# Optimization experiments

Hardware: AMD Instinct MI355X
Metric: run time of the kernel (lower is better)

## Reference

```python
import jax, jax.numpy as jnp
import numpy as np

N = 100000
E = 1600000
IN_DIM = 128
HID = 128
OUT_DIM = 64
ORDER = 4


def setup_inputs() -> dict:
    key = jax.random.key(0)
    ks = jax.random.split(key, 10)
    x = jax.random.normal(ks[0], (N, IN_DIM), dtype=jnp.float32)
    edge_index = jax.random.randint(ks[1], (2, E), 0, N, dtype=jnp.int64)
    gen_edge_index = jax.random.randint(ks[2], (2, E), 0, N, dtype=jnp.int64)
    s = 1.0 / np.sqrt(IN_DIM)
    w_orig = jax.random.normal(ks[3], (ORDER + 1, IN_DIM, HID), dtype=jnp.float32) * s
    b_orig = jax.random.normal(ks[4], (ORDER + 1, HID), dtype=jnp.float32) * s
    w_aug = jax.random.normal(ks[5], (ORDER + 1, IN_DIM, HID), dtype=jnp.float32) * s
    b_aug = jax.random.normal(ks[6], (ORDER + 1, HID), dtype=jnp.float32) * s
    fusion_weight = jnp.ones((2,), dtype=jnp.float32)
    clf_w = jax.random.normal(ks[7], (HID, OUT_DIM), dtype=jnp.float32) / np.sqrt(HID)
    clf_b = jax.random.normal(ks[8], (OUT_DIM,), dtype=jnp.float32) / np.sqrt(HID)
    return {"x": x, "edge_index": edge_index, "gen_edge_index": gen_edge_index,
            "w_orig": w_orig, "b_orig": b_orig, "w_aug": w_aug, "b_aug": b_aug,
            "fusion_weight": fusion_weight, "clf_w": clf_w, "clf_b": clf_b}


def _beta_wavelet(x, edge_index, W, b, num_nodes):
    # add self loops
    loop = jnp.arange(num_nodes, dtype=edge_index.dtype)
    row = jnp.concatenate([edge_index[0], loop])
    col = jnp.concatenate([edge_index[1], loop])
    # symmetric normalization D^{-1/2} A D^{-1/2}
    deg = jax.ops.segment_sum(jnp.ones_like(col, dtype=x.dtype), col, num_segments=num_nodes)
    dinv = jnp.where(deg > 0, deg ** -0.5, 0.0)
    norm = dinv[row] * dinv[col]  # [E+N]
    out = x @ W[0] + b[0]
    Tx = x
    for i in range(1, ORDER + 1):
        msg = norm[:, None] * Tx[row]                      # gather + scale [E+N, D]
        Tx = jax.ops.segment_sum(msg, col, num_segments=num_nodes)  # scatter_add
        out = out + Tx @ W[i] + b[i]
    return jax.nn.relu(out)


def reference(x, edge_index, gen_edge_index, w_orig, b_orig, w_aug, b_aug, fusion_weight, clf_w, clf_b):
    num_nodes = x.shape[0]
    h_orig = _beta_wavelet(x, edge_index, w_orig, b_orig, num_nodes)
    h_aug = _beta_wavelet(x, gen_edge_index, w_aug, b_aug, num_nodes)
    w = jax.nn.softmax(fusion_weight)
    h_final = w[0] * h_orig + w[1] * h_aug
    return h_final @ clf_w + clf_b
```

## Files before the change

### kernel.cpp

```cpp
#include <hip/hip_runtime.h>

#define N_NODES 100000
#define NPAD    100096
#define NE      1600000
#define DIM     128
#define ODIM    64
#define NORDER  4
#define NB      391
#define PB_EDGES 16384
#define PB_BLKS  98

typedef _Float16 h8 __attribute__((ext_vector_type(8)));
typedef float f4 __attribute__((ext_vector_type(4)));

__device__ __forceinline__ float2 up2(unsigned p) {
    union { unsigned u; _Float16 h[2]; } c; c.u = p;
    return make_float2((float)c.h[0], (float)c.h[1]);
}
__device__ __forceinline__ unsigned pk2(float x, float y) {
    union { unsigned u; _Float16 h[2]; } c;
    c.h[0] = (_Float16)x; c.h[1] = (_Float16)y;
    return c.u;
}
__device__ __forceinline__ unsigned short f2hbits(float x) {
    union { _Float16 h; unsigned short s; } c;
    c.h = (_Float16)x;
    return c.s;
}
__device__ __forceinline__ float h2f(unsigned short s) {
    union { unsigned short u; _Float16 h; } c;
    c.u = s;
    return (float)c.h;
}

__global__ __launch_bounds__(256) void hist_edges(const int* __restrict__ e0,
                                                  const int* __restrict__ e1,
                                                  int* __restrict__ bhist) {
    __shared__ int lh[NB];
    int t = threadIdx.x;
    int g = blockIdx.x >= 782;
    int blk = g ? (blockIdx.x - 782) : blockIdx.x;
    const int* colp = (g ? e1 : e0) + NE;
    int* bh = bhist + g * NB;
    for (int i = t; i < NB; i += 256) lh[i] = 0;
    __syncthreads();
    int base = blk * 2048 + t;
#pragma unroll
    for (int j = 0; j < 8; ++j) {
        int e = base + j * 256;
        if (e < NE) atomicAdd(&lh[colp[e] >> 8], 1);
    }
    __syncthreads();
    for (int i = t; i < NB; i += 256) if (lh[i]) atomicAdd(&bh[i], lh[i]);
}

__global__ void wave_scan(const int* __restrict__ in,
                          int* __restrict__ oexcl,
                          int* __restrict__ ocur,
                          int n) {
    int wv = threadIdx.x >> 6, lane = threadIdx.x & 63;
    if (wv >= 2) return;
    const int* I = in + wv * n;
    int* O = oexcl + wv * (n + 1);
    int* C = ocur + wv * n;
    int carry = 0;
    for (int base = 0; base < n; base += 64) {
        int i = base + lane;
        int v = (i < n) ? I[i] : 0;
        int s = v;
#pragma unroll
        for (int off = 1; off < 64; off <<= 1) {
            int x = __shfl_up(s, off, 64);
            if (lane >= off) s += x;
        }
        int excl = carry + s - v;
        if (i < n) {
            O[i] = excl;
            C[i] = excl;
        }
        carry += __shfl(s, 63, 64);
    }
    if (lane == 0) O[n] = carry;
}

__global__ __launch_bounds__(1024) void part_edges(const int* __restrict__ e0,
                                                   const int* __restrict__ e1,
                                                   int* __restrict__ bcursor,
                                                   unsigned* __restrict__ pairs) {
    __shared__ int lh[NB];
    __shared__ int lpos[NB];
    int t = threadIdx.x;
    int g = blockIdx.x >= PB_BLKS;
    int blk = g ? (blockIdx.x - PB_BLKS) : blockIdx.x;
    const int* rowp = (g ? e1 : e0);
    const int* colp = rowp + NE;
    int* bc = bcursor + g * NB;
    unsigned* pr = pairs + (size_t)g * NE;
    for (int i = t; i < NB; i += 1024) lh[i] = 0;
    __syncthreads();
    int base = blk * PB_EDGES + t;
    int rank[16];
    short bk[16];
    unsigned char lcv[16];
#pragma unroll
    for (int j = 0; j < 16; ++j) {
        int e = base + j * 1024;
        rank[j] = -1;
        if (e < NE) {
            int c = colp[e];
            bk[j] = (short)(c >> 8);
            lcv[j] = (unsigned char)(c & 255);
            rank[j] = atomicAdd(&lh[c >> 8], 1);
        }
    }
    __syncthreads();
    for (int i = t; i < NB; i += 1024) {
        int n = lh[i];
        lpos[i] = n ? atomicAdd(&bc[i], n) : 0;
    }
    __syncthreads();
#pragma unroll
    for (int j = 0; j < 16; ++j) {
        int e = base + j * 1024;
        if (e < NE) {
            int b = bk[j];
            pr[lpos[b] + rank[j]] = ((unsigned)rowp[e] << 8) | lcv[j];
        }
    }
}

__global__ __launch_bounds__(256) void bucket_csr(const unsigned* __restrict__ pairs,
                                                  const int* __restrict__ boff,
                                                  int* __restrict__ ptrv,
                                                  float* __restrict__ dinv,
                                                  int* __restrict__ srcv) {
    __shared__ int lcnt[256];
    __shared__ int lbase[256];
    int t = threadIdx.x;
    int g = blockIdx.x >= NB;
    int b = g ? (blockIdx.x - NB) : blockIdx.x;
    const unsigned* pr = pairs + (size_t)g * NE;
    const int* bo = boff + g * (NB + 1);
    int* pv = ptrv + g * (N_NODES + 1);
    float* dv = dinv + g * N_NODES;
    int* sv = srcv + (size_t)g * NE;
    lcnt[t] = 0;
    __syncthreads();
    int s = bo[b], e = bo[b + 1];
    for (int i = s + t; i < e; i += 256)
        atomicAdd(&lcnt[pr[i] & 255u], 1);
    __syncthreads();
    int v = lcnt[t];
    lbase[t] = v;
    __syncthreads();
    for (int off = 1; off < 256; off <<= 1) {
        int x = (t >= off) ? lbase[t - off] : 0;
        __syncthreads();
        lbase[t] += x;
        __syncthreads();
    }
    int node = (b << 8) + t;
    int gbase = s + lbase[t] - v;
    lbase[t] = gbase;
    lcnt[t] = 0;
    if (node < N_NODES) {
        pv[node] = gbase;
        dv[node] = rsqrtf((float)(v + 1));
    }
    if (b == 0 && g == 0 && t == 0) ptrv[N_NODES] = NE;
    if (b == 0 && g == 1 && t == 0) ptrv[2 * N_NODES + 1] = NE;
    __syncthreads();
    for (int i = s + t; i < e; i += 256) {
        unsigned pk = pr[i];
        int lc = (int)(pk & 255u);
        int pos = lbase[lc] + atomicAdd(&lcnt[lc], 1);
        sv[pos] = (int)(pk >> 8);
    }
}

__global__ __launch_bounds__(256) void s0cast(const float* __restrict__ x,
                                              const float* __restrict__ dinv,
                                              unsigned* __restrict__ S0o,
                                              unsigned* __restrict__ S0a) {
    int idx = blockIdx.x * 256 + threadIdx.x;
    if (idx >= NPAD * 64) return;
    int m = idx >> 6, u = idx & 63;
    if (m < N_NODES) {
        int e = (m << 7) + u * 2;
        float a = x[e], b = x[e + 1];
        float d0 = dinv[m];
        float d1 = dinv[N_NODES + m];
        S0o[idx] = pk2(d0 * a, d0 * b);
        S0a[idx] = pk2(d1 * a, d1 * b);
    } else {
        S0o[idx] = 0u;
        S0a[idx] = 0u;
    }
}

__global__ __launch_bounds__(256) void wcast(const float* __restrict__ Wo,
                                             const float* __restrict__ Wa,
                                             const float* __restrict__ cw,
                                             const float* __restrict__ bO,
                                             const float* __restrict__ bA,
                                             const float* __restrict__ fw,
                                             unsigned short* __restrict__ Wt,
                                             float* __restrict__ params) {
    int idx = blockIdx.x * 256 + threadIdx.x;
    if (idx >= 2 * 5 * DIM * DIM + ODIM * DIM) return;
    if (idx < 258) {
        if (idx < 2) {
            float f0 = fw[0], f1 = fw[1];
            float mx = fmaxf(f0, f1);
            float e0 = expf(f0 - mx), e1 = expf(f1 - mx);
            params[idx] = (idx == 0 ? e0 : e1) / (e0 + e1);
        } else if (idx < 130) {
            int n = idx - 2;
            float s = 0.f;
            for (int i = 0; i <= NORDER; ++i) s += bO[i * DIM + n];
            params[idx] = s;
        } else {
            int n = idx - 130;
            float s = 0.f;
            for (int i = 0; i <= NORDER; ++i) s += bA[i * DIM + n];
            params[idx] = s;
        }
    }
    if (idx < 2 * 5 * DIM * DIM) {
        int g   = idx / (5 * DIM * DIM);
        int rem = idx % (5 * DIM * DIM);
        int i   = rem / (DIM * DIM);
        int r2  = rem % (DIM * DIM);
        int k8  = r2 >> 10;
        int n   = (r2 >> 3) & 127;
        int k7  = r2 & 7;
        int k   = k8 * 8 + k7;
        const float* W = g ? Wa : Wo;
        Wt[idx] = f2hbits(W[(i * DIM + k) * DIM + n]);
    } else {
        int j = idx - 2 * 5 * DIM * DIM;
        int n = j >> 7, k = j & 127;
        Wt[idx] = f2hbits(cw[k * ODIM + n]);
    }
}

template<int SIN>
__global__ __launch_bounds__(256) void propagate(const unsigned* __restrict__ Tin,
                                                 unsigned* __restrict__ Tout,
                                                 const int* __restrict__ ptrv,
                                                 const int* __restrict__ srcv,
                                                 const float* __restrict__ dinv) {
    int gid  = blockIdx.x * 256 + threadIdx.x;
    int lane = threadIdx.x & 63;
    int v    = __builtin_amdgcn_readfirstlane(gid >> 6);
    if (v >= N_NODES) return;
    float dv = dinv[v];
    float2 self = up2(Tin[(size_t)v * SIN + lane]);
    float ax = self.x, ay = self.y;
    int beg = ptrv[v], end = ptrv[v + 1];
    for (int k = beg; k < end; k += 16) {
        int u[16];
#pragma unroll
        for (int j = 0; j < 16; ++j) {
            int e  = k + j;
            int su = srcv[e < NE ? e : (NE - 1)];
            u[j]   = (e < end) ? su : N_NODES;
        }
        unsigned tw[16];
#pragma unroll
        for (int j = 0; j < 16; ++j)
            tw[j] = Tin[(size_t)((unsigned)u[j] * SIN) + lane];
#pragma unroll
        for (int j = 0; j < 16; ++j) {
            float2 t = up2(tw[j]);
            ax += t.x; ay += t.y;
        }
    }
    float s2 = dv * dv;
    Tout[(size_t)v * 256 + lane] = pk2(s2 * ax, s2 * ay);
}

__global__ __launch_bounds__(256, 2) void gemmH0(
        const unsigned short* __restrict__ A0,
        const unsigned short* __restrict__ A,
        const unsigned short* __restrict__ Wt,
        const float* __restrict__ params,
        const float* __restrict__ dinv,
        unsigned short* __restrict__ H0) {
    int t = threadIdx.x;
    int lane = t & 63, wv = t >> 6;
    int m0 = blockIdx.x * 128 + wv * 32;
    int l15 = lane & 15, q = lane >> 4;
    float sw0 = params[0];
    float bs[8];
#pragma unroll
    for (int nt = 0; nt < 8; ++nt) bs[nt] = params[2 + nt * 16 + l15];

    f4 acc[2][8];
#pragma unroll
    for (int mt = 0; mt < 2; ++mt)
#pragma unroll
        for (int nt = 0; nt < 8; ++nt) acc[mt][nt] = (f4)(0.f);

#pragma unroll
    for (int i = 0; i < 5; ++i) {
        const unsigned short* WtI = Wt + (size_t)i * DIM * DIM;
        const unsigned short* Ai = (i == 0) ? A0 : (A + (size_t)(i - 1) * DIM);
        const int rs = (i == 0) ? DIM : 512;
        h8 af[2][4];
#pragma unroll
        for (int mt = 0; mt < 2; ++mt)
#pragma unroll
            for (int kc = 0; kc < 4; ++kc)
                af[mt][kc] = *(const h8*)(Ai + (size_t)(m0 + mt * 16 + l15) * rs
                                             + (kc * 4 + q) * 8);
#pragma unroll
        for (int kc = 0; kc < 4; ++kc) {
            int c = kc * 4 + q;
#pragma unroll
            for (int nt = 0; nt < 8; ++nt) {
                h8 bf = *(const h8*)(WtI + (size_t)(c * 128 + nt * 16 + l15) * 8);
                acc[0][nt] = __builtin_amdgcn_mfma_f32_16x16x32_f16(af[0][kc], bf, acc[0][nt], 0, 0, 0);
                acc[1][nt] = __builtin_amdgcn_mfma_f32_16x16x32_f16(af[1][kc], bf, acc[1][nt], 0, 0, 0);
            }
        }
    }
#pragma unroll
    for (int mt = 0; mt < 2; ++mt) {
        float rd[4];
#pragma unroll
        for (int r = 0; r < 4; ++r) {
            int row = m0 + mt * 16 + q * 4 + r;
            rd[r] = 1.0f / dinv[row < N_NODES ? row : (N_NODES - 1)];
        }
#pragma unroll
        for (int nt = 0; nt < 8; ++nt) {
#pragma unroll
            for (int r = 0; r < 4; ++r) {
                int row = m0 + mt * 16 + q * 4 + r;
                H0[(size_t)row * DIM + nt * 16 + l15] =
                    f2hbits(sw0 * fmaxf(rd[r] * acc[mt][nt][r] + bs[nt], 0.f));
            }
        }
    }
}

__global__ __launch_bounds__(256, 2) void gemm_fused2(
        const unsigned short* __restrict__ A0,
        const unsigned short* __restrict__ A,
        const unsigned short* __restrict__ Wt,
        const unsigned short* __restrict__ H0,
        const float* __restrict__ params,
        const float* __restrict__ dinv,
        const unsigned short* __restrict__ clfWt,
        const float* __restrict__ clfB,
        float* __restrict__ out) {
    __shared__ unsigned short Hl[DIM * 132];
    int t = threadIdx.x;
    int lane = t & 63, wv = t >> 6;
    int mb = blockIdx.x * 128;
    int m0 = mb + wv * 32;
    int l15 = lane & 15, q = lane >> 4;
    float sw1 = params[1];
    float bs[8];
#pragma unroll
    for (int nt = 0; nt < 8; ++nt) bs[nt] = params[130 + nt * 16 + l15];

    f4 acc[2][8];
#pragma unroll
    for (int mt = 0; mt < 2; ++mt)
#pragma unroll
        for (int nt = 0; nt < 8; ++nt) acc[mt][nt] = (f4)(0.f);

#pragma unroll
    for (int i = 0; i < 5; ++i) {
        const unsigned short* WtI = Wt + (size_t)i * DIM * DIM;
        const unsigned short* Ai = (i == 0) ? A0 : (A + (size_t)(i - 1) * DIM);
        const int rs = (i == 0) ? DIM : 512;
        h8 af[2][4];
#pragma unroll
        for (int mt = 0; mt < 2; ++mt)
#pragma unroll
            for (int kc = 0; kc < 4; ++kc)
                af[mt][kc] = *(const h8*)(Ai + (size_t)(m0 + mt * 16 + l15) * rs
                                             + (kc * 4 + q) * 8);
#pragma unroll
        for (int kc = 0; kc < 4; ++kc) {
            int c = kc * 4 + q;
#pragma unroll
            for (int nt = 0; nt < 8; ++nt) {
                h8 bf = *(const h8*)(WtI + (size_t)(c * 128 + nt * 16 + l15) * 8);
                acc[0][nt] = __builtin_amdgcn_mfma_f32_16x16x32_f16(af[0][kc], bf, acc[0][nt], 0, 0, 0);
                acc[1][nt] = __builtin_amdgcn_mfma_f32_16x16x32_f16(af[1][kc], bf, acc[1][nt], 0, 0, 0);
            }
        }
    }

#pragma unroll
    for (int j = 0; j < 8; ++j) {
        int chunk = t + j * 256;
        int row = chunk >> 4, c8 = chunk & 15;
        *(h8*)&Hl[row * 132 + c8 * 8] =
            *(const h8*)&H0[(size_t)(mb + row) * DIM + c8 * 8];
    }
    __syncthreads();

#pragma unroll
    for (int mt = 0; mt < 2; ++mt) {
        float rd[4];
#pragma unroll
        for (int r = 0; r < 4; ++r) {
            int row = m0 + mt * 16 + q * 4 + r;
            rd[r] = 1.0f / dinv[row < N_NODES ? row : (N_NODES - 1)];
        }
#pragma unroll
        for (int nt = 0; nt < 8; ++nt) {
            int col = nt * 16 + l15;
#pragma unroll
            for (int r = 0; r < 4; ++r) {
                int lrow = wv * 32 + mt * 16 + q * 4 + r;
                float h = sw1 * fmaxf(rd[r] * acc[mt][nt][r] + bs[nt], 0.f)
                        + h2f(Hl[lrow * 132 + col]);
                Hl[lrow * 132 + col] = f2hbits(h);
            }
        }
    }
    __syncthreads();

    f4 o[2][4];
#pragma unroll
    for (int mt = 0; mt < 2; ++mt)
#pragma unroll
        for (int n2 = 0; n2 < 4; ++n2) o[mt][n2] = (f4)(0.f);
#pragma unroll
    for (int kc = 0; kc < 4; ++kc) {
        int c = kc * 4 + q;
        h8 ha[2];
#pragma unroll
        for (int mt = 0; mt < 2; ++mt)
            ha[mt] = *(const h8*)&Hl[(wv * 32 + mt * 16 + l15) * 132 + c * 8];
#pragma unroll
        for (int n2 = 0; n2 < 4; ++n2) {
            h8 bf = *(const h8*)&clfWt[(size_t)(n2 * 16 + l15) * DIM + c * 8];
            o[0][n2] = __builtin_amdgcn_mfma_f32_16x16x32_f16(ha[0], bf, o[0][n2], 0, 0, 0);
            o[1][n2] = __builtin_amdgcn_mfma_f32_16x16x32_f16(ha[1], bf, o[1][n2], 0, 0, 0);
        }
    }
#pragma unroll
    for (int mt = 0; mt < 2; ++mt)
#pragma unroll
        for (int n2 = 0; n2 < 4; ++n2) {
            int col = n2 * 16 + l15;
            float cbv = clfB[col];
#pragma unroll
            for (int r = 0; r < 4; ++r) {
                int row = m0 + mt * 16 + q * 4 + r;
                if (row < N_NODES) out[(size_t)row * ODIM + col] = o[mt][n2][r] + cbv;
            }
        }
}

extern "C" void kernel_launch(void* const* d_in, const int* in_sizes, int n_in,
                              void* d_out, int out_size, void* d_ws, size_t ws_size,
                              hipStream_t stream) {
    const float* x   = (const float*)d_in[0];
    const int*   ei  = (const int*)d_in[1];
    const int*   gi  = (const int*)d_in[2];
    const float* w_o = (const float*)d_in[3];
    const float* b_o = (const float*)d_in[4];
    const float* w_a = (const float*)d_in[5];
    const float* b_a = (const float*)d_in[6];
    const float* fw  = (const float*)d_in[7];
    const float* cw  = (const float*)d_in[8];
    const float* cb  = (const float*)d_in[9];
    float* out = (float*)d_out;

    char* p = (char*)d_ws;
    auto alloc = [&](size_t bytes) {
        void* r = (void*)p;
        p += (bytes + 255) & ~(size_t)255;
        return r;
    };
    unsigned* Tbig = (unsigned*)alloc((size_t)NPAD * 256 * 4);
    unsigned* S0o  = (unsigned*)alloc((size_t)NPAD * 64 * 4);
    unsigned* S0a  = (unsigned*)alloc((size_t)NPAD * 64 * 4);
    unsigned short* H0 = (unsigned short*)alloc((size_t)NPAD * DIM * 2);
    unsigned short* Wt = (unsigned short*)alloc(((size_t)2 * 5 * DIM * DIM + ODIM * DIM) * 2);
    float* params = (float*)alloc(258 * 4);
    float* dinv  = (float*)alloc((size_t)2 * N_NODES * 4);
    unsigned* pairs = (unsigned*)alloc((size_t)2 * NE * 4);
    int* csr_src = (int*)alloc((size_t)2 * NE * 4);
    int* csr_ptr = (int*)alloc((size_t)2 * (N_NODES + 1) * 4);
    int* bhist   = (int*)alloc((size_t)2 * NB * 4);
    int* boff    = (int*)alloc((size_t)2 * (NB + 1) * 4);
    int* bcursor = (int*)alloc((size_t)2 * NB * 4);

    const int gP  = (N_NODES * 64 + 255) / 256;
    const int gX  = (NPAD * 64 + 255) / 256;
    const int gW  = (2 * 5 * DIM * DIM + ODIM * DIM + 255) / 256;
    const int gM  = NPAD / 128;

    hipMemsetAsync(Tbig + (size_t)N_NODES * 256, 0,
                   (size_t)(NPAD - N_NODES) * 256 * 4, stream);
    hipMemsetAsync(bhist, 0, (size_t)2 * NB * 4, stream);

    wcast<<<gW, 256, 0, stream>>>(w_o, w_a, cw, b_o, b_a, fw, Wt, params);

    hist_edges<<<2 * 782, 256, 0, stream>>>(ei, gi, bhist);
    wave_scan<<<1, 128, 0, stream>>>(bhist, boff, bcursor, NB);
    part_edges<<<2 * PB_BLKS, 1024, 0, stream>>>(ei, gi, bcursor, pairs);
    bucket_csr<<<2 * NB, 256, 0, stream>>>(pairs, boff, csr_ptr, dinv, csr_src);

    s0cast<<<gX, 256, 0, stream>>>(x, dinv, S0o, S0a);

    propagate<64><<<gP, 256, 0, stream>>>(S0o, Tbig, csr_ptr, csr_src, dinv);
    propagate<256><<<gP, 256, 0, stream>>>(Tbig, Tbig + 64, csr_ptr, csr_src, dinv);
    propagate<256><<<gP, 256, 0, stream>>>(Tbig + 64, Tbig + 128, csr_ptr, csr_src, dinv);
    propagate<256><<<gP, 256, 0, stream>>>(Tbig + 128, Tbig + 192, csr_ptr, csr_src, dinv);
    gemmH0<<<gM, 256, 0, stream>>>((const unsigned short*)S0o, (const unsigned short*)Tbig,
                                   Wt, params, dinv, H0);

    {
        const int* pv = csr_ptr + (N_NODES + 1);
        const int* sv = csr_src + (size_t)NE;
        const float* dv = dinv + (size_t)N_NODES;
        propagate<64><<<gP, 256, 0, stream>>>(S0a, Tbig, pv, sv, dv);
        propagate<256><<<gP, 256, 0, stream>>>(Tbig, Tbig + 64, pv, sv, dv);
        propagate<256><<<gP, 256, 0, stream>>>(Tbig + 64, Tbig + 128, pv, sv, dv);
        propagate<256><<<gP, 256, 0, stream>>>(Tbig + 128, Tbig + 192, pv, sv, dv);
    }
    gemm_fused2<<<gM, 256, 0, stream>>>((const unsigned short*)S0a,
                                        (const unsigned short*)Tbig,
                                        Wt + (size_t)5 * DIM * DIM,
                                        H0, params, dinv + N_NODES,
                                        Wt + (size_t)2 * 5 * DIM * DIM, cb, out);
}
```

Before: 899.8 us.

## Double-buffer weight tiles in LDS via async global-to-LDS loads in fused GEMMs

Both MFMA GEMM kernels now stage each order's 128x128 fp16 weight tile into a double-buffered LDS array using global_load_lds async copies, prefetching the next order's weights and A fragments while computing the current one. Previously B fragments were read directly from global memory inside the inner MFMA loop. The fused kernel reuses the LDS buffer for the H tile and reads H0 directly from global memory instead of staging it. This raises LDS use to 64KB per block, which may reduce occupancy below the requested two blocks per CU, and it adds barriers per order.

```diff
diff --git a/kernel.cpp b/kernel.cpp
--- a/kernel.cpp
+++ b/kernel.cpp
@@ -31,6 +31,10 @@
     union { unsigned short u; _Float16 h; } c;
     c.u = s;
     return (float)c.h;
+}
+__device__ __forceinline__ void async_cp16(const void* g, void* l) {
+    __builtin_amdgcn_global_load_lds((const __attribute__((address_space(1))) void*)g,
+                                     (__attribute__((address_space(3))) void*)l, 16, 0, 0);
 }
 
 __global__ __launch_bounds__(256) void hist_edges(const int* __restrict__ e0,
@@ -287,6 +291,7 @@
         const float* __restrict__ params,
         const float* __restrict__ dinv,
         unsigned short* __restrict__ H0) {
+    __shared__ unsigned short Bl[2][DIM * DIM];
     int t = threadIdx.x;
     int lane = t & 63, wv = t >> 6;
     int m0 = blockIdx.x * 128 + wv * 32;
@@ -302,28 +307,50 @@
 #pragma unroll
         for (int nt = 0; nt < 8; ++nt) acc[mt][nt] = (f4)(0.f);
 
+    h8 af[2][2][4];
+
+#pragma unroll
+    for (int c = 0; c < 8; ++c) {
+        int ci = c * 4 + wv;
+        async_cp16(Wt + ci * 512 + lane * 8, &Bl[0][ci * 512]);
+    }
+#pragma unroll
+    for (int mt = 0; mt < 2; ++mt)
+#pragma unroll
+        for (int kc = 0; kc < 4; ++kc)
+            af[0][mt][kc] = *(const h8*)(A0 + (size_t)(m0 + mt * 16 + l15) * DIM
+                                            + (kc * 4 + q) * 8);
+    __syncthreads();
+
 #pragma unroll
     for (int i = 0; i < 5; ++i) {
-        const unsigned short* WtI = Wt + (size_t)i * DIM * DIM;
-        const unsigned short* Ai = (i == 0) ? A0 : (A + (size_t)(i - 1) * DIM);
-        const int rs = (i == 0) ? DIM : 512;
-        h8 af[2][4];
-#pragma unroll
-        for (int mt = 0; mt < 2; ++mt)
-#pragma unroll
-            for (int kc = 0; kc < 4; ++kc)
-                af[mt][kc] = *(const h8*)(Ai + (size_t)(m0 + mt * 16 + l15) * rs
-                                             + (kc * 4 + q) * 8);
+        if (i < 4) {
+            const unsigned short* WtN = Wt + (size_t)(i + 1) * DIM * DIM;
+#pragma unroll
+            for (int c = 0; c < 8; ++c) {
+                int ci = c * 4 + wv;
+                async_cp16(WtN + ci * 512 + lane * 8, &Bl[(i & 1) ^ 1][ci * 512]);
+            }
+            const unsigned short* AiN = A + (size_t)i * DIM;
+#pragma unroll
+            for (int mt = 0; mt < 2; ++mt)
+#pragma unroll
+                for (int kc = 0; kc < 4; ++kc)
+                    af[(i & 1) ^ 1][mt][kc] =
+                        *(const h8*)(AiN + (size_t)(m0 + mt * 16 + l15) * 512
+                                        + (kc * 4 + q) * 8);
+        }
 #pragma unroll
         for (int kc = 0; kc < 4; ++kc) {
             int c = kc * 4 + q;
 #pragma unroll
             for (int nt = 0; nt < 8; ++nt) {
-                h8 bf = *(const h8*)(WtI + (size_t)(c * 128 + nt * 16 + l15) * 8);
-                acc[0][nt] = __builtin_amdgcn_mfma_f32_16x16x32_f16(af[0][kc], bf, acc[0][nt], 0, 0, 0);
-                acc[1][nt] = __builtin_amdgcn_mfma_f32_16x16x32_f16(af[1][kc], bf, acc[1][nt], 0, 0, 0);
-            }
-        }
+                h8 bf = *(const h8*)&Bl[i & 1][(size_t)(c * 128 + nt * 16 + l15) * 8];
+                acc[0][nt] = __builtin_amdgcn_mfma_f32_16x16x32_f16(af[i & 1][0][kc], bf, acc[0][nt], 0, 0, 0);
+                acc[1][nt] = __builtin_amdgcn_mfma_f32_16x16x32_f16(af[i & 1][1][kc], bf, acc[1][nt], 0, 0, 0);
+            }
+        }
+        if (i < 4) __syncthreads();
     }
 #pragma unroll
     for (int mt = 0; mt < 2; ++mt) {
@@ -355,11 +382,11 @@
         const unsigned short* __restrict__ clfWt,
         const float* __restrict__ clfB,
         float* __restrict__ out) {
-    __shared__ unsigned short Hl[DIM * 132];
+    __shared__ unsigned short Bl[2][DIM * DIM];
+    unsigned short* Hl = &Bl[0][0];
     int t = threadIdx.x;
     int lane = t & 63, wv = t >> 6;
-    int mb = blockIdx.x * 128;
-    int m0 = mb + wv * 32;
+    int m0 = blockIdx.x * 128 + wv * 32;
     int l15 = lane & 15, q = lane >> 4;
     float sw1 = params[1];
     float bs[8];
@@ -372,38 +399,51 @@
 #pragma unroll
         for (int nt = 0; nt < 8; ++nt) acc[mt][nt] = (f4)(0.f);
 
+    h8 af[2][2][4];
+
+#pragma unroll
+    for (int c = 0; c < 8; ++c) {
+        int ci = c * 4 + wv;
+        async_cp16(Wt + ci * 512 + lane * 8, &Bl[0][ci * 512]);
+    }
+#pragma unroll
+    for (int mt = 0; mt < 2; ++mt)
+#pragma unroll
+        for (int kc = 0; kc < 4; ++kc)
+            af[0][mt][kc] = *(const h8*)(A0 + (size_t)(m0 + mt * 16 + l15) * DIM
+                                            + (kc * 4 + q) * 8);
+    __syncthreads();
+
 #pragma unroll
     for (int i = 0; i < 5; ++i) {
-        const unsigned short* WtI = Wt + (size_t)i * DIM * DIM;
-        const unsigned short* Ai = (i == 0) ? A0 : (A + (size_t)(i - 1) * DIM);
-        const int rs = (i == 0) ? DIM : 512;
-        h8 af[2][4];
-#pragma unroll
-        for (int mt = 0; mt < 2; ++mt)
-#pragma unroll
-            for (int kc = 0; kc < 4; ++kc)
-                af[mt][kc] = *(const h8*)(Ai + (size_t)(m0 + mt * 16 + l15) * rs
-                                             + (kc * 4 + q) * 8);
+        if (i < 4) {
+            const unsigned short* WtN = Wt + (size_t)(i + 1) * DIM * DIM;
+#pragma unroll
+            for (int c = 0; c < 8; ++c) {
+                int ci = c * 4 + wv;
+                async_cp16(WtN + ci * 512 + lane * 8, &Bl[(i & 1) ^ 1][ci * 512]);
+            }
+            const unsigned short* AiN = A + (size_t)i * DIM;
+#pragma unroll
+            for (int mt = 0; mt < 2; ++mt)
+#pragma unroll
+                for (int kc = 0; kc < 4; ++kc)
+                    af[(i & 1) ^ 1][mt][kc] =
+                        *(const h8*)(AiN + (size_t)(m0 + mt * 16 + l15) * 512
+                                        + (kc * 4 + q) * 8);
+        }
 #pragma unroll
         for (int kc = 0; kc < 4; ++kc) {
             int c = kc * 4 + q;
 #pragma unroll
             for (int nt = 0; nt < 8; ++nt) {
-                h8 bf = *(const h8*)(WtI + (size_t)(c * 128 + nt * 16 + l15) * 8);
-                acc[0][nt] = __builtin_amdgcn_mfma_f32_16x16x32_f16(af[0][kc], bf, acc[0][nt], 0, 0, 0);
-                acc[1][nt] = __builtin_amdgcn_mfma_f32_16x16x32_f16(af[1][kc], bf, acc[1][nt], 0, 0, 0);
-            }
-        }
-    }
-
-#pragma unroll
-    for (int j = 0; j < 8; ++j) {
-        int chunk = t + j * 256;
-        int row = chunk >> 4, c8 = chunk & 15;
-        *(h8*)&Hl[row * 132 + c8 * 8] =
-            *(const h8*)&H0[(size_t)(mb + row) * DIM + c8 * 8];
-    }
-    __syncthreads();
+                h8 bf = *(const h8*)&Bl[i & 1][(size_t)(c * 128 + nt * 16 + l15) * 8];
+                acc[0][nt] = __builtin_amdgcn_mfma_f32_16x16x32_f16(af[i & 1][0][kc], bf, acc[0][nt], 0, 0, 0);
+                acc[1][nt] = __builtin_amdgcn_mfma_f32_16x16x32_f16(af[i & 1][1][kc], bf, acc[1][nt], 0, 0, 0);
+            }
+        }
+        __syncthreads();
+    }
 
 #pragma unroll
     for (int mt = 0; mt < 2; ++mt) {
@@ -419,8 +459,9 @@
 #pragma unroll
             for (int r = 0; r < 4; ++r) {
                 int lrow = wv * 32 + mt * 16 + q * 4 + r;
+                int grow = m0 + mt * 16 + q * 4 + r;
                 float h = sw1 * fmaxf(rd[r] * acc[mt][nt][r] + bs[nt], 0.f)
-                        + h2f(Hl[lrow * 132 + col]);
+                        + h2f(H0[(size_t)grow * DIM + col]);
                 Hl[lrow * 132 + col] = f2hbits(h);
             }
         }
```

Result: faster. 785.7 us (-12.7%).

## Batch both graphs' propagation per launch and stage GEMM weights in LDS

Applied to the files above, without the earlier changes.

When the workspace is large enough, each propagation order now runs for the original and the augmented graph in a single launch, with a separate T buffer per graph and the pairs scratch aliased onto the second T buffer. This halves the number of propagation launches and doubles the blocks per wave of work. Both GEMM kernels now copy each weight slice into shared memory with async global-to-LDS loads, and gemmH0 occupancy is raised to 3. The host memsets move into existing kernels, and gemm_fused2 reads H0 directly from global memory. The extra barriers and the doubled buffer footprint could raise cache pressure.

```diff
diff --git a/kernel.cpp b/kernel.cpp
--- a/kernel.cpp
+++ b/kernel.cpp
@@ -9,9 +9,11 @@
 #define NB      391
 #define PB_EDGES 16384
 #define PB_BLKS  98
+#define GPB     25000
 
 typedef _Float16 h8 __attribute__((ext_vector_type(8)));
 typedef float f4 __attribute__((ext_vector_type(4)));
+typedef unsigned u4v __attribute__((ext_vector_type(4)));
 
 __device__ __forceinline__ float2 up2(unsigned p) {
     union { unsigned u; _Float16 h[2]; } c; c.u = p;
@@ -31,6 +33,10 @@
     union { unsigned short u; _Float16 h; } c;
     c.u = s;
     return (float)c.h;
+}
+__device__ __forceinline__ void async_cp16(const void* g, void* l) {
+    __builtin_amdgcn_global_load_lds((const __attribute__((address_space(1))) void*)g,
+                                     (__attribute__((address_space(3))) void*)l, 16, 0, 0);
 }
 
 __global__ __launch_bounds__(256) void hist_edges(const int* __restrict__ e0,
@@ -181,7 +187,9 @@
 __global__ __launch_bounds__(256) void s0cast(const float* __restrict__ x,
                                               const float* __restrict__ dinv,
                                               unsigned* __restrict__ S0o,
-                                              unsigned* __restrict__ S0a) {
+                                              unsigned* __restrict__ S0a,
+                                              unsigned* __restrict__ To,
+                                              unsigned* __restrict__ Ta) {
     int idx = blockIdx.x * 256 + threadIdx.x;
     if (idx >= NPAD * 64) return;
     int m = idx >> 6, u = idx & 63;
@@ -195,6 +203,9 @@
     } else {
         S0o[idx] = 0u;
         S0a[idx] = 0u;
+        u4v z = (u4v)(0u);
+        *(u4v*)&To[(size_t)m * 256 + u * 4] = z;
+        *(u4v*)&Ta[(size_t)m * 256 + u * 4] = z;
     }
 }
 
@@ -205,9 +216,11 @@
                                              const float* __restrict__ bA,
                                              const float* __restrict__ fw,
                                              unsigned short* __restrict__ Wt,
-                                             float* __restrict__ params) {
+                                             float* __restrict__ params,
+                                             int* __restrict__ bhist) {
     int idx = blockIdx.x * 256 + threadIdx.x;
     if (idx >= 2 * 5 * DIM * DIM + ODIM * DIM) return;
+    if (idx < 2 * NB) bhist[idx] = 0;
     if (idx < 258) {
         if (idx < 2) {
             float f0 = fw[0], f1 = fw[1];
@@ -245,25 +258,35 @@
 }
 
 template<int SIN>
-__global__ __launch_bounds__(256) void propagate(const unsigned* __restrict__ Tin,
-                                                 unsigned* __restrict__ Tout,
-                                                 const int* __restrict__ ptrv,
-                                                 const int* __restrict__ srcv,
-                                                 const float* __restrict__ dinv) {
-    int gid  = blockIdx.x * 256 + threadIdx.x;
+__global__ __launch_bounds__(256) void propagate2(const unsigned* __restrict__ T0i,
+                                                  unsigned* __restrict__ T0o,
+                                                  const unsigned* __restrict__ T1i,
+                                                  unsigned* __restrict__ T1o,
+                                                  const int* __restrict__ ptrv,
+                                                  const int* __restrict__ srcv,
+                                                  const float* __restrict__ dinv) {
+    int bid = blockIdx.x;
+    int g = bid >= GPB;
+    bid -= g * GPB;
+    const unsigned* Tin = g ? T1i : T0i;
+    unsigned* Tout      = g ? T1o : T0o;
+    const int* pv   = ptrv + g * (N_NODES + 1);
+    const int* sv   = srcv + (size_t)g * NE;
+    const float* dp = dinv + g * N_NODES;
+    int gid  = bid * 256 + threadIdx.x;
     int lane = threadIdx.x & 63;
     int v    = __builtin_amdgcn_readfirstlane(gid >> 6);
     if (v >= N_NODES) return;
-    float dv = dinv[v];
+    float dv = dp[v];
     float2 self = up2(Tin[(size_t)v * SIN + lane]);
     float ax = self.x, ay = self.y;
-    int beg = ptrv[v], end = ptrv[v + 1];
+    int beg = pv[v], end = pv[v + 1];
     for (int k = beg; k < end; k += 16) {
         int u[16];
 #pragma unroll
         for (int j = 0; j < 16; ++j) {
             int e  = k + j;
-            int su = srcv[e < NE ? e : (NE - 1)];
+            int su = sv[e < NE ? e : (NE - 1)];
             u[j]   = (e < end) ? su : N_NODES;
         }
         unsigned tw[16];
@@ -280,13 +303,14 @@
     Tout[(size_t)v * 256 + lane] = pk2(s2 * ax, s2 * ay);
 }
 
-__global__ __launch_bounds__(256, 2) void gemmH0(
+__global__ __launch_bounds__(256, 3) void gemmH0(
         const unsigned short* __restrict__ A0,
         const unsigned short* __restrict__ A,
         const unsigned short* __restrict__ Wt,
         const float* __restrict__ params,
         const float* __restrict__ dinv,
         unsigned short* __restrict__ H0) {
+    __shared__ unsigned short Bl[DIM * DIM];
     int t = threadIdx.x;
     int lane = t & 63, wv = t >> 6;
     int m0 = blockIdx.x * 128 + wv * 32;
@@ -315,15 +339,22 @@
                 af[mt][kc] = *(const h8*)(Ai + (size_t)(m0 + mt * 16 + l15) * rs
                                              + (kc * 4 + q) * 8);
 #pragma unroll
+        for (int c = 0; c < 8; ++c) {
+            int ci = c * 4 + wv;
+            async_cp16(WtI + ci * 512 + lane * 8, &Bl[ci * 512]);
+        }
+        __syncthreads();
+#pragma unroll
         for (int kc = 0; kc < 4; ++kc) {
             int c = kc * 4 + q;
 #pragma unroll
             for (int nt = 0; nt < 8; ++nt) {
-                h8 bf = *(const h8*)(WtI + (size_t)(c * 128 + nt * 16 + l15) * 8);
+                h8 bf = *(const h8*)&Bl[(size_t)(c * 128 + nt * 16 + l15) * 8];
                 acc[0][nt] = __builtin_amdgcn_mfma_f32_16x16x32_f16(af[0][kc], bf, acc[0][nt], 0, 0, 0);
                 acc[1][nt] = __builtin_amdgcn_mfma_f32_16x16x32_f16(af[1][kc], bf, acc[1][nt], 0, 0, 0);
             }
         }
+        __syncthreads();
     }
 #pragma unroll
     for (int mt = 0; mt < 2; ++mt) {
@@ -355,11 +386,12 @@
         const unsigned short* __restrict__ clfWt,
         const float* __restrict__ clfB,
         float* __restrict__ out) {
-    __shared__ unsigned short Hl[DIM * 132];
+    __shared__ unsigned short BlH[DIM * 132];
+    unsigned short* Bl = BlH;
+    unsigned short* Hl = BlH;
     int t = threadIdx.x;
     int lane = t & 63, wv = t >> 6;
-    int mb = blockIdx.x * 128;
-    int m0 = mb + wv * 32;
+    int m0 = blockIdx.x * 128 + wv * 32;
     int l15 = lane & 15, q = lane >> 4;
     float sw1 = params[1];
     float bs[8];
@@ -385,25 +417,23 @@
                 af[mt][kc] = *(const h8*)(Ai + (size_t)(m0 + mt * 16 + l15) * rs
                                              + (kc * 4 + q) * 8);
 #pragma unroll
+        for (int c = 0; c < 8; ++c) {
+            int ci = c * 4 + wv;
+            async_cp16(WtI + ci * 512 + lane * 8, &Bl[ci * 512]);
+        }
+        __syncthreads();
+#pragma unroll
         for (int kc = 0; kc < 4; ++kc) {
             int c = kc * 4 + q;
 #pragma unroll
             for (int nt = 0; nt < 8; ++nt) {
-                h8 bf = *(const h8*)(WtI + (size_t)(c * 128 + nt * 16 + l15) * 8);
+                h8 bf = *(const h8*)&Bl[(size_t)(c * 128 + nt * 16 + l15) * 8];
                 acc[0][nt] = __builtin_amdgcn_mfma_f32_16x16x32_f16(af[0][kc], bf, acc[0][nt], 0, 0, 0);
                 acc[1][nt] = __builtin_amdgcn_mfma_f32_16x16x32_f16(af[1][kc], bf, acc[1][nt], 0, 0, 0);
             }
         }
-    }
-
-#pragma unroll
-    for (int j = 0; j < 8; ++j) {
-        int chunk = t + j * 256;
-        int row = chunk >> 4, c8 = chunk & 15;
-        *(h8*)&Hl[row * 132 + c8 * 8] =
-            *(const h8*)&H0[(size_t)(mb + row) * DIM + c8 * 8];
-    }
-    __syncthreads();
+        __syncthreads();
+    }
 
 #pragma unroll
     for (int mt = 0; mt < 2; ++mt) {
@@ -419,8 +449,9 @@
 #pragma unroll
             for (int r = 0; r < 4; ++r) {
                 int lrow = wv * 32 + mt * 16 + q * 4 + r;
+                int grow = m0 + mt * 16 + q * 4 + r;
                 float h = sw1 * fmaxf(rd[r] * acc[mt][nt][r] + bs[nt], 0.f)
-                        + h2f(Hl[lrow * 132 + col]);
+                        + h2f(H0[(size_t)grow * DIM + col]);
                 Hl[lrow * 132 + col] = f2hbits(h);
             }
         }
@@ -475,63 +506,107 @@
     const float* cb  = (const float*)d_in[9];
     float* out = (float*)d_out;
 
+    auto align256 = [](size_t b) { return (b + 255) & ~(size_t)255; };
+    const size_t szTbig = (size_t)NPAD * 256 * 4;
+    const size_t szS0   = (size_t)NPAD * 64 * 4;
+    const size_t szH0   = (size_t)NPAD * DIM * 2;
+    const size_t szWt   = ((size_t)2 * 5 * DIM * DIM + ODIM * DIM) * 2;
+    const size_t szPar  = 258 * 4;
+    const size_t szDinv = (size_t)2 * N_NODES * 4;
+    const size_t szPairs= (size_t)2 * NE * 4;
+    const size_t szSrc  = (size_t)2 * NE * 4;
+    const size_t szPtr  = (size_t)2 * (N_NODES + 1) * 4;
+    const size_t szBh   = (size_t)2 * NB * 4;
+    const size_t szBo   = (size_t)2 * (NB + 1) * 4;
+
+    const size_t needBig = align256(szTbig) * 2 + align256(szS0) * 2 + align256(szH0)
+                         + align256(szWt) + align256(szPar) + align256(szDinv)
+                         + align256(szSrc) + align256(szPtr) + align256(szBh) * 2
+                         + align256(szBo);
+    const bool big = (ws_size >= needBig);
+
     char* p = (char*)d_ws;
     auto alloc = [&](size_t bytes) {
         void* r = (void*)p;
         p += (bytes + 255) & ~(size_t)255;
         return r;
     };
-    unsigned* Tbig = (unsigned*)alloc((size_t)NPAD * 256 * 4);
-    unsigned* S0o  = (unsigned*)alloc((size_t)NPAD * 64 * 4);
-    unsigned* S0a  = (unsigned*)alloc((size_t)NPAD * 64 * 4);
-    unsigned short* H0 = (unsigned short*)alloc((size_t)NPAD * DIM * 2);
-    unsigned short* Wt = (unsigned short*)alloc(((size_t)2 * 5 * DIM * DIM + ODIM * DIM) * 2);
-    float* params = (float*)alloc(258 * 4);
-    float* dinv  = (float*)alloc((size_t)2 * N_NODES * 4);
-    unsigned* pairs = (unsigned*)alloc((size_t)2 * NE * 4);
-    int* csr_src = (int*)alloc((size_t)2 * NE * 4);
-    int* csr_ptr = (int*)alloc((size_t)2 * (N_NODES + 1) * 4);
-    int* bhist   = (int*)alloc((size_t)2 * NB * 4);
-    int* boff    = (int*)alloc((size_t)2 * (NB + 1) * 4);
-    int* bcursor = (int*)alloc((size_t)2 * NB * 4);
-
-    const int gP  = (N_NODES * 64 + 255) / 256;
+    unsigned* Tbig_o = (unsigned*)alloc(szTbig);
+    unsigned* Tbig_a = big ? (unsigned*)alloc(szTbig) : Tbig_o;
+    unsigned* pairs  = big ? Tbig_a : (unsigned*)alloc(szPairs);
+    unsigned* S0o  = (unsigned*)alloc(szS0);
+    unsigned* S0a  = (unsigned*)alloc(szS0);
+    unsigned short* H0 = (unsigned short*)alloc(szH0);
+    unsigned short* Wt = (unsigned short*)alloc(szWt);
+    float* params = (float*)alloc(szPar);
+    float* dinv  = (float*)alloc(szDinv);
+    int* csr_src = (int*)alloc(szSrc);
+    int* csr_ptr = (int*)alloc(szPtr);
+    int* bhist   = (int*)alloc(szBh);
+    int* boff    = (int*)alloc(szBo);
+    int* bcursor = (int*)alloc(szBh);
+
     const int gX  = (NPAD * 64 + 255) / 256;
     const int gW  = (2 * 5 * DIM * DIM + ODIM * DIM + 255) / 256;
     const int gM  = NPAD / 128;
 
-    hipMemsetAsync(Tbig + (size_t)N_NODES * 256, 0,
-                   (size_t)(NPAD - N_NODES) * 256 * 4, stream);
-    hipMemsetAsync(bhist, 0, (size_t)2 * NB * 4, stream);
-
-    wcast<<<gW, 256, 0, stream>>>(w_o, w_a, cw, b_o, b_a, fw, Wt, params);
+    wcast<<<gW, 256, 0, stream>>>(w_o, w_a, cw, b_o, b_a, fw, Wt, params, bhist);
 
     hist_edges<<<2 * 782, 256, 0, stream>>>(ei, gi, bhist);
     wave_scan<<<1, 128, 0, stream>>>(bhist, boff, bcursor, NB);
     part_edges<<<2 * PB_BLKS, 1024, 0, stream>>>(ei, gi, bcursor, pairs);
     bucket_csr<<<2 * NB, 256, 0, stream>>>(pairs, boff, csr_ptr, dinv, csr_src);
 
-    s0cast<<<gX, 256, 0, stream>>>(x, dinv, S0o, S0a);
-
-    propagate<64><<<gP, 256, 0, stream>>>(S0o, Tbig, csr_ptr, csr_src, dinv);
-    propagate<256><<<gP, 256, 0, stream>>>(Tbig, Tbig + 64, csr_ptr, csr_src, dinv);
-    propagate<256><<<gP, 256, 0, stream>>>(Tbig + 64, Tbig + 128, csr_ptr, csr_src, dinv);
-    propagate<256><<<gP, 256, 0, stream>>>(Tbig + 128, Tbig + 192, csr_ptr, csr_src, dinv);
-    gemmH0<<<gM, 256, 0, stream>>>((const unsigned short*)S0o, (const unsigned short*)Tbig,
-                                   Wt, params, dinv, H0);
-
-    {
+    s0cast<<<gX, 256, 0, stream>>>(x, dinv, S0o, S0a, Tbig_o, Tbig_a);
+
+    if (big) {
+        propagate2<64><<<2 * GPB, 256, 0, stream>>>(S0o, Tbig_o, S0a, Tbig_a,
+                                                    csr_ptr, csr_src, dinv);
+        propagate2<256><<<2 * GPB, 256, 0, stream>>>(Tbig_o, Tbig_o + 64,
+                                                     Tbig_a, Tbig_a + 64,
+                                                     csr_ptr, csr_src, dinv);
+        propagate2<256><<<2 * GPB, 256, 0, stream>>>(Tbig_o + 64, Tbig_o + 128,
+                                                     Tbig_a + 64, Tbig_a + 128,
+                                                     csr_ptr, csr_src, dinv);
+        propagate2<256><<<2 * GPB, 256, 0, stream>>>(Tbig_o + 128, Tbig_o + 192,
+                                                     Tbig_a + 128, Tbig_a + 192,
+                                                     csr_ptr, csr_src, dinv);
+        gemmH0<<<gM, 256, 0, stream>>>((const unsigned short*)S0o,
+                                       (const unsigned short*)Tbig_o,
+                                       Wt, params, dinv, H0);
+        gemm_fused2<<<gM, 256, 0, stream>>>((const unsigned short*)S0a,
+                                            (const unsigned short*)Tbig_a,
+                                            Wt + (size_t)5 * DIM * DIM,
+                                            H0, params, dinv + N_NODES,
+                                            Wt + (size_t)2 * 5 * DIM * DIM, cb, out);
+    } else {
+        propagate2<64><<<GPB, 256, 0, stream>>>(S0o, Tbig_o, S0o, Tbig_o,
+                                                csr_ptr, csr_src, dinv);
+        propagate2<256><<<GPB, 256, 0, stream>>>(Tbig_o, Tbig_o + 64, Tbig_o, Tbig_o + 64,
+                                                 csr_ptr, csr_src, dinv);
+        propagate2<256><<<GPB, 256, 0, stream>>>(Tbig_o + 64, Tbig_o + 128,
+                                                 Tbig_o + 64, Tbig_o + 128,
+                                                 csr_ptr, csr_src, dinv);
+        propagate2<256><<<GPB, 256, 0, stream>>>(Tbig_o + 128, Tbig_o + 192,
+                                                 Tbig_o + 128, Tbig_o + 192,
+                                                 csr_ptr, csr_src, dinv);
+        gemmH0<<<gM, 256, 0, stream>>>((const unsigned short*)S0o,
+                                       (const unsigned short*)Tbig_o,
+                                       Wt, params, dinv, H0);
         const int* pv = csr_ptr + (N_NODES + 1);
         const int* sv = csr_src + (size_t)NE;
         const float* dv = dinv + (size_t)N_NODES;
-        propagate<64><<<gP, 256, 0, stream>>>(S0a, Tbig, pv, sv, dv);
-        propagate<256><<<gP, 256, 0, stream>>>(Tbig, Tbig + 64, pv, sv, dv);
-        propagate<256><<<gP, 256, 0, stream>>>(Tbig + 64, Tbig + 128, pv, sv, dv);
-        propagate<256><<<gP, 256, 0, stream>>>(Tbig + 128, Tbig + 192, pv, sv, dv);
-    }
-    gemm_fused2<<<gM, 256, 0, stream>>>((const unsigned short*)S0a,
-                                        (const unsigned short*)Tbig,
-                                        Wt + (size_t)5 * DIM * DIM,
-                                        H0, params, dinv + N_NODES,
-                                        Wt + (size_t)2 * 5 * DIM * DIM, cb, out);
-}
+        propagate2<64><<<GPB, 256, 0, stream>>>(S0a, Tbig_o, S0a, Tbig_o, pv, sv, dv);
+        propagate2<256><<<GPB, 256, 0, stream>>>(Tbig_o, Tbig_o + 64, Tbig_o, Tbig_o + 64,
+                                                 pv, sv, dv);
+        propagate2<256><<<GPB, 256, 0, stream>>>(Tbig_o + 64, Tbig_o + 128,
+                                                 Tbig_o + 64, Tbig_o + 128, pv, sv, dv);
+        propagate2<256><<<GPB, 256, 0, stream>>>(Tbig_o + 128, Tbig_o + 192,
+                                                 Tbig_o + 128, Tbig_o + 192, pv, sv, dv);
+        gemm_fused2<<<gM, 256, 0, stream>>>((const unsigned short*)S0a,
+                                            (const unsigned short*)Tbig_o,
+                                            Wt + (size_t)5 * DIM * DIM,
+                                            H0, params, dinv + N_NODES,
+                                            Wt + (size_t)2 * 5 * DIM * DIM, cb, out);
+    }
+}
```

After: 776.2 us. -13.7%, faster.
